# Kernel tuning notes

Measured on AMD Instinct MI355X. Metric: run time of the kernel, lower is better.

## Reference

```python
import jax, jax.numpy as jnp
import numpy as np

B, T, D, H = 32, 2048, 256, 256

def setup_inputs() -> dict:
    key = jax.random.key(0)
    k1, k2, k3 = jax.random.split(key, 3)
    s_x = 1.0 / np.sqrt(D)
    s_h = 1.0 / np.sqrt(H)
    return {
        "x": jax.random.normal(k1, (B, T, D), dtype=jnp.float32),
        "W_x": jax.random.normal(k2, (D, 3 * H), dtype=jnp.float32) * s_x,
        "W_h": jax.random.normal(k3, (H, 3 * H), dtype=jnp.float32) * s_h,
        "b": jnp.zeros((3 * H,), dtype=jnp.float32),
    }

def reference(x, W_x, W_h, b):
    # GRU cell unrolled over time; state starts at zeros (reset_state=True).
    # Precompute input projections for all timesteps in one big GEMM: [B,T,3H]
    x_proj = jnp.einsum("btd,dg->btg", x, W_x) + b
    h0 = jnp.zeros((x.shape[0], H), dtype=x.dtype)

    def step(h, xp_t):
        xz, xr, xn = jnp.split(xp_t, 3, axis=-1)          # each [B,H]
        hz, hr, hn = jnp.split(h @ W_h, 3, axis=-1)        # each [B,H]
        z = jax.nn.sigmoid(xz + hz)
        r = jax.nn.sigmoid(xr + hr)
        n = jnp.tanh(xn + r * hn)
        h_new = z * h + (1.0 - z) * n
        return h_new, h_new

    # scan over time (axis 1 -> move to leading axis)
    _, ys = jax.lax.scan(step, h0, jnp.swapaxes(x_proj, 0, 1))
    return jnp.swapaxes(ys, 0, 1)  # [B,T,H]
```

## Files before the change

kernel.cpp:

```cpp
#include <hip/hip_runtime.h>

#define Bb 32
#define Tt 2048
#define Dd 256
#define Hh 256
#define G3 768

typedef _Float16 h2_t __attribute__((ext_vector_type(2)));
typedef _Float16 f16x8 __attribute__((ext_vector_type(8)));
typedef float f32x4 __attribute__((ext_vector_type(4)));
union H2U { unsigned u; _Float16 h[2]; h2_t v; };
union V16 { uint4 u; f16x8 f; };

__device__ __forceinline__ float fdot2f(unsigned a, unsigned b, float c) {
#if __has_builtin(__builtin_amdgcn_fdot2)
    H2U ua, ub; ua.u = a; ub.u = b;
    return __builtin_amdgcn_fdot2(ua.v, ub.v, c, false);
#else
    H2U ua, ub; ua.u = a; ub.u = b;
    return c + (float)ua.h[0] * (float)ub.h[0] + (float)ua.h[1] * (float)ub.h[1];
#endif
}

__device__ __forceinline__ float frcpf(float x) {
#if __has_builtin(__builtin_amdgcn_rcpf)
    return __builtin_amdgcn_rcpf(x);
#else
    return 1.0f / x;
#endif
}
__device__ __forceinline__ float sigmoidf_(float s) { return frcpf(1.0f + __expf(-s)); }
__device__ __forceinline__ float tanhf_(float u) {
    float e = __expf(2.0f * u);
    return 1.0f - 2.0f * frcpf(e + 1.0f);
}
__device__ __forceinline__ float dpp_xor1(float v) {
    return __int_as_float(__builtin_amdgcn_update_dpp(0, __float_as_int(v), 0xB1, 0xF, 0xF, true));
}
__device__ __forceinline__ float dpp_xor2(float v) {
    return __int_as_float(__builtin_amdgcn_update_dpp(0, __float_as_int(v), 0x4E, 0xF, 0xF, true));
}

__global__ void cvt_x_kernel(const float* __restrict__ x, _Float16* __restrict__ xo) {
    const size_t i = ((size_t)blockIdx.x * 256 + threadIdx.x) * 4;
    float4 v = *reinterpret_cast<const float4*>(x + i);
    H2U a, b;
    a.h[0] = (_Float16)v.x; a.h[1] = (_Float16)v.y;
    b.h[0] = (_Float16)v.z; b.h[1] = (_Float16)v.w;
    uint2 o; o.x = a.u; o.y = b.u;
    *reinterpret_cast<uint2*>(xo + i) = o;
}

__global__ void wxt_kernel(const float* __restrict__ Wx, _Float16* __restrict__ wxt) {
    const int o = blockIdx.x * 256 + threadIdx.x;
    const int n = o >> 7, kp = o & 127;
    float f0 = Wx[(size_t)(2 * kp) * G3 + n];
    float f1 = Wx[(size_t)(2 * kp + 1) * G3 + n];
    H2U u; u.h[0] = (_Float16)f0; u.h[1] = (_Float16)f1;
    reinterpret_cast<unsigned*>(wxt)[o] = u.u;
}

__global__ __launch_bounds__(256)
void gemm_xp_kernel(const _Float16* __restrict__ A, const _Float16* __restrict__ Bm,
                    const float* __restrict__ bias, _Float16* __restrict__ xp) {
    __shared__ _Float16 As[128][264];
    __shared__ _Float16 Bs[64][264];
    const int tid = threadIdx.x;
    const int m0 = (blockIdx.x / 12) * 128;
    const int n0 = (blockIdx.x % 12) * 64;

#pragma unroll
    for (int it = 0; it < 16; ++it) {
        int c = tid + it * 256, row = c >> 5, col = c & 31;
        uint4 v = *reinterpret_cast<const uint4*>(A + (size_t)(m0 + row) * 256 + col * 8);
        *reinterpret_cast<uint4*>(&As[row][col * 8]) = v;
    }
#pragma unroll
    for (int it = 0; it < 8; ++it) {
        int c = tid + it * 256, row = c >> 5, col = c & 31;
        uint4 v = *reinterpret_cast<const uint4*>(Bm + (size_t)(n0 + row) * 256 + col * 8);
        *reinterpret_cast<uint4*>(&Bs[row][col * 8]) = v;
    }
    __syncthreads();

    const int wave = tid >> 6, lane = tid & 63;
    const int wr = wave >> 1, wc = wave & 1;
    const int r16 = lane & 15, kg = lane >> 4;

    f32x4 acc[4][2];
#pragma unroll
    for (int mi = 0; mi < 4; ++mi)
#pragma unroll
        for (int ni = 0; ni < 2; ++ni) acc[mi][ni] = (f32x4){0.f, 0.f, 0.f, 0.f};

    float bv[2];
#pragma unroll
    for (int ni = 0; ni < 2; ++ni) bv[ni] = bias[n0 + wc * 32 + ni * 16 + r16];

#pragma unroll
    for (int kk = 0; kk < 8; ++kk) {
        f16x8 a[4], b2[2];
#pragma unroll
        for (int mi = 0; mi < 4; ++mi) {
            V16 t; t.u = *reinterpret_cast<const uint4*>(&As[wr * 64 + mi * 16 + r16][kk * 32 + kg * 8]);
            a[mi] = t.f;
        }
#pragma unroll
        for (int ni = 0; ni < 2; ++ni) {
            V16 t; t.u = *reinterpret_cast<const uint4*>(&Bs[wc * 32 + ni * 16 + r16][kk * 32 + kg * 8]);
            b2[ni] = t.f;
        }
#pragma unroll
        for (int mi = 0; mi < 4; ++mi)
#pragma unroll
            for (int ni = 0; ni < 2; ++ni)
                acc[mi][ni] = __builtin_amdgcn_mfma_f32_16x16x32_f16(a[mi], b2[ni], acc[mi][ni], 0, 0, 0);
    }

#pragma unroll
    for (int mi = 0; mi < 4; ++mi)
#pragma unroll
        for (int ni = 0; ni < 2; ++ni)
#pragma unroll
            for (int r = 0; r < 4; ++r) {
                int row = m0 + wr * 64 + mi * 16 + kg * 4 + r;
                int col = n0 + wc * 32 + ni * 16 + r16;
                xp[(size_t)row * G3 + col] = (_Float16)(acc[mi][ni][r] + bv[ni]);
            }
}

#define GDOT(HF)                                                                      \
  {                                                                                   \
    uint4 h0 = hq[(HF) * 2 + 0];                                                      \
    uint4 h1 = hq[(HF) * 2 + 1];                                                      \
    _Pragma("unroll") for (int u = 0; u < 4; ++u) {                                   \
      const unsigned hu = (u == 0) ? h0.x : (u == 1) ? h0.y : (u == 2) ? h0.z : h0.w; \
      sz0 = fdot2f(w[0][0][(HF) * 8 + u], hu, sz0);                                   \
      sr0 = fdot2f(w[1][0][(HF) * 8 + u], hu, sr0);                                   \
      sn0 = fdot2f(w[2][0][(HF) * 8 + u], hu, sn0);                                   \
      sz1 = fdot2f(w[0][1][(HF) * 8 + u], hu, sz1);                                   \
      sr1 = fdot2f(w[1][1][(HF) * 8 + u], hu, sr1);                                   \
      sn1 = fdot2f(w[2][1][(HF) * 8 + u], hu, sn1);                                   \
    }                                                                                 \
    _Pragma("unroll") for (int u = 0; u < 4; ++u) {                                   \
      const unsigned hu = (u == 0) ? h1.x : (u == 1) ? h1.y : (u == 2) ? h1.z : h1.w; \
      sz0 = fdot2f(w[0][0][(HF) * 8 + 4 + u], hu, sz0);                               \
      sr0 = fdot2f(w[1][0][(HF) * 8 + 4 + u], hu, sr0);                               \
      sn0 = fdot2f(w[2][0][(HF) * 8 + 4 + u], hu, sn0);                               \
      sz1 = fdot2f(w[0][1][(HF) * 8 + 4 + u], hu, sz1);                               \
      sr1 = fdot2f(w[1][1][(HF) * 8 + 4 + u], hu, sr1);                               \
      sn1 = fdot2f(w[2][1][(HF) * 8 + 4 + u], hu, sn1);                               \
    }                                                                                 \
  }

#define GSTEP(PR, PW, T)                                                              \
  {                                                                                   \
              \
                   \
    const _Float16* xnp = xq + (size_t)((T) + 1 < Tt ? (T) + 1 : (T)) * G3;           \
    _Float16 pz = xnp[0], pr = xnp[Hh], pn = xnp[2 * Hh];                             \
    float sz0 = 0.f, sz1 = 0.f, sr0 = 0.f, sr1 = 0.f, sn0 = 0.f, sn1 = 0.f;           \
    const uint4* hq = reinterpret_cast<const uint4*>(&hbuf[PR][q * 36]);              \
    GDOT(0) GDOT(1) GDOT(2) GDOT(3)                                                   \
                                \
    sz0 += dpp_xor1(sz0); sz1 += dpp_xor1(sz1);                                       \
    sr0 += dpp_xor1(sr0); sr1 += dpp_xor1(sr1);                                       \
    sn0 += dpp_xor1(sn0); sn1 += dpp_xor1(sn1);                                       \
    sz0 += dpp_xor2(sz0); sz1 += dpp_xor2(sz1);                                       \
    sr0 += dpp_xor2(sr0); sr1 += dpp_xor2(sr1);                                       \
    sn0 += dpp_xor2(sn0); sn1 += dpp_xor2(sn1);                                       \
    const float hz = (q & 1) ? sz1 : sz0;                                             \
    const float hr = (q & 1) ? sr1 : sr0;                                             \
    const float hn = (q & 1) ? sn1 : sn0;                                             \
    const float zg = sigmoidf_(xz + hz);                                              \
    const float rg = sigmoidf_(xr + hr);                                              \
    const float ng = tanhf_(xn + rg * hn);                                            \
    const float hnew = zg * hprev + (1.0f - zg) * ng;                                 \
    hprev = hnew;                                                                     \
    H2U hc; hc.h[0] = (_Float16)hnew; hc.h[1] = (_Float16)0.f;                        \
    const unsigned pu = (unsigned)__builtin_amdgcn_update_dpp(0, (int)hc.u, 0xB1, 0xF, 0xF, true); \
    const int pf = __builtin_amdgcn_update_dpp(0, __float_as_int(hnew), 0xB1, 0xF, 0xF, true);      \
    if (q == 0) {                                                                     \
      hbuf[PW][(slot >> 5) * 36 + (slot & 31)] = (hc.u & 0xFFFFu) | (pu << 16);       \
      float2 yv; yv.x = hnew; yv.y = __int_as_float(pf);                              \
      *reinterpret_cast<float2*>(yb + (size_t)(T) * Hh) = yv;                         \
    }                                                                                 \
    xz = (float)pz; xr = (float)pr; xn = (float)pn;                                   \
    __builtin_amdgcn_sched_barrier(0);                                                \
    asm volatile("s_waitcnt lgkmcnt(0)" ::: "memory");                                \
    __builtin_amdgcn_s_barrier();                                                     \
    __builtin_amdgcn_sched_barrier(0);                                                \
  }

__global__ __launch_bounds__(512, 2)
void gru_scan_kernel(const _Float16* __restrict__ xp, const float* __restrict__ Wh,
                     float* __restrict__ y) {
    __shared__ unsigned hbuf[2][144];

    const int tid = threadIdx.x;
    const int b = blockIdx.x;
    const int q = tid & 3;
    const int slot = tid >> 2;

    unsigned w[3][2][32];
#pragma unroll
    for (int g = 0; g < 3; ++g) {
        const int c0 = g * Hh + 2 * slot;
#pragma unroll
        for (int kp = 0; kp < 32; ++kp) {
            const int k = 64 * q + 2 * kp;
            float2 f0 = *reinterpret_cast<const float2*>(Wh + (size_t)k * G3 + c0);
            float2 f1 = *reinterpret_cast<const float2*>(Wh + (size_t)(k + 1) * G3 + c0);
            H2U p0, p1;
            p0.h[0] = (_Float16)f0.x; p0.h[1] = (_Float16)f1.x;
            p1.h[0] = (_Float16)f0.y; p1.h[1] = (_Float16)f1.y;
            w[g][0][kp] = p0.u;
            w[g][1][kp] = p1.u;
        }
    }

    if (tid < 288) hbuf[tid / 144][tid % 144] = 0u;
    float hprev = 0.0f;

    const int j = 2 * slot + (q & 1);
    const _Float16* xq = xp + (size_t)b * Tt * G3 + j;
    float* yb = y + (size_t)b * Tt * Hh + 2 * slot;
    float xz = (float)xq[0], xr = (float)xq[Hh], xn = (float)xq[2 * Hh];

    __syncthreads();

#pragma unroll 1
    for (int t = 0; t < Tt; t += 2) {
        GSTEP(0, 1, t);
        GSTEP(1, 0, t + 1);
    }
}

extern "C" void kernel_launch(void* const* d_in, const int* in_sizes, int n_in,
                              void* d_out, int out_size, void* d_ws, size_t ws_size,
                              hipStream_t stream) {
    (void)in_sizes; (void)n_in; (void)out_size; (void)ws_size;
    const float* x    = (const float*)d_in[0];
    const float* Wx   = (const float*)d_in[1];
    const float* Wh   = (const float*)d_in[2];
    const float* bias = (const float*)d_in[3];
    float* y = (float*)d_out;

    _Float16* xp   = (_Float16*)d_ws;
    _Float16* xf16 = (_Float16*)d_out;
    _Float16* wxt  = (_Float16*)((char*)d_out + (size_t)33554432);

    cvt_x_kernel<<<dim3(16384), dim3(256), 0, stream>>>(x, xf16);
    wxt_kernel<<<dim3(384), dim3(256), 0, stream>>>(Wx, wxt);
    gemm_xp_kernel<<<dim3(6144), dim3(256), 0, stream>>>(xf16, wxt, bias, xp);
    gru_scan_kernel<<<dim3(Bb), dim3(512), 0, stream>>>(xp, Wh, y);
}
```

Baseline: 2.190 ms.

## Halve scan block to 256 threads, each thread computing four hidden columns

The recurrent scan kernel now uses 256 threads per batch row instead of 512. Each thread holds weights for four output columns across all three gates (384 registers), computes 12 partial dot products per step, and owns one hidden unit. This removes the dpp pair exchange for writing h and y and the software prefetch of the next step's input projection. Fewer waves per barrier shortens the per-step synchronisation, but it doubles per-thread FMA work and register pressure, which risks spills and a longer serial step.

Result: slower. 6.281 ms (+186.8%).

```diff
diff --git a/kernel.cpp b/kernel.cpp
--- a/kernel.cpp
+++ b/kernel.cpp
@@ -129,70 +129,60 @@
             }
 }
 
-#define GDOT(HF)                                                                      \
+#define GDCOL(HU, KP)                                                                 \
+    az0 = fdot2f(w[0][0][KP], HU, az0); ar0 = fdot2f(w[1][0][KP], HU, ar0);           \
+    an0 = fdot2f(w[2][0][KP], HU, an0); az1 = fdot2f(w[0][1][KP], HU, az1);           \
+    ar1 = fdot2f(w[1][1][KP], HU, ar1); an1 = fdot2f(w[2][1][KP], HU, an1);           \
+    az2 = fdot2f(w[0][2][KP], HU, az2); ar2 = fdot2f(w[1][2][KP], HU, ar2);           \
+    an2 = fdot2f(w[2][2][KP], HU, an2); az3 = fdot2f(w[0][3][KP], HU, az3);           \
+    ar3 = fdot2f(w[1][3][KP], HU, ar3); an3 = fdot2f(w[2][3][KP], HU, an3);
+
+#define GD4(I)                                                                        \
   {                                                                                   \
-    uint4 h0 = hq[(HF) * 2 + 0];                                                      \
-    uint4 h1 = hq[(HF) * 2 + 1];                                                      \
-    _Pragma("unroll") for (int u = 0; u < 4; ++u) {                                   \
-      const unsigned hu = (u == 0) ? h0.x : (u == 1) ? h0.y : (u == 2) ? h0.z : h0.w; \
-      sz0 = fdot2f(w[0][0][(HF) * 8 + u], hu, sz0);                                   \
-      sr0 = fdot2f(w[1][0][(HF) * 8 + u], hu, sr0);                                   \
-      sn0 = fdot2f(w[2][0][(HF) * 8 + u], hu, sn0);                                   \
-      sz1 = fdot2f(w[0][1][(HF) * 8 + u], hu, sz1);                                   \
-      sr1 = fdot2f(w[1][1][(HF) * 8 + u], hu, sr1);                                   \
-      sn1 = fdot2f(w[2][1][(HF) * 8 + u], hu, sn1);                                   \
-    }                                                                                 \
-    _Pragma("unroll") for (int u = 0; u < 4; ++u) {                                   \
-      const unsigned hu = (u == 0) ? h1.x : (u == 1) ? h1.y : (u == 2) ? h1.z : h1.w; \
-      sz0 = fdot2f(w[0][0][(HF) * 8 + 4 + u], hu, sz0);                               \
-      sr0 = fdot2f(w[1][0][(HF) * 8 + 4 + u], hu, sr0);                               \
-      sn0 = fdot2f(w[2][0][(HF) * 8 + 4 + u], hu, sn0);                               \
-      sz1 = fdot2f(w[0][1][(HF) * 8 + 4 + u], hu, sz1);                               \
-      sr1 = fdot2f(w[1][1][(HF) * 8 + 4 + u], hu, sr1);                               \
-      sn1 = fdot2f(w[2][1][(HF) * 8 + 4 + u], hu, sn1);                               \
-    }                                                                                 \
+    uint4 hv = hq[I];                                                                 \
+    GDCOL(hv.x, (I) * 4 + 0)                                                          \
+    GDCOL(hv.y, (I) * 4 + 1)                                                          \
+    GDCOL(hv.z, (I) * 4 + 2)                                                          \
+    GDCOL(hv.w, (I) * 4 + 3)                                                          \
   }
 
 #define GSTEP(PR, PW, T)                                                              \
   {                                                                                   \
               \
-                   \
-    const _Float16* xnp = xq + (size_t)((T) + 1 < Tt ? (T) + 1 : (T)) * G3;           \
-    _Float16 pz = xnp[0], pr = xnp[Hh], pn = xnp[2 * Hh];                             \
-    float sz0 = 0.f, sz1 = 0.f, sr0 = 0.f, sr1 = 0.f, sn0 = 0.f, sn1 = 0.f;           \
+    const _Float16* xt = xq + (size_t)(T) * G3;                                       \
+    const _Float16 xgz = xt[0], xgr = xt[Hh], xgn = xt[2 * Hh];                       \
+    float az0 = 0.f, az1 = 0.f, az2 = 0.f, az3 = 0.f;                                 \
+    float ar0 = 0.f, ar1 = 0.f, ar2 = 0.f, ar3 = 0.f;                                 \
+    float an0 = 0.f, an1 = 0.f, an2 = 0.f, an3 = 0.f;                                 \
     const uint4* hq = reinterpret_cast<const uint4*>(&hbuf[PR][q * 36]);              \
-    GDOT(0) GDOT(1) GDOT(2) GDOT(3)                                                   \
-                                \
-    sz0 += dpp_xor1(sz0); sz1 += dpp_xor1(sz1);                                       \
-    sr0 += dpp_xor1(sr0); sr1 += dpp_xor1(sr1);                                       \
-    sn0 += dpp_xor1(sn0); sn1 += dpp_xor1(sn1);                                       \
-    sz0 += dpp_xor2(sz0); sz1 += dpp_xor2(sz1);                                       \
-    sr0 += dpp_xor2(sr0); sr1 += dpp_xor2(sr1);                                       \
-    sn0 += dpp_xor2(sn0); sn1 += dpp_xor2(sn1);                                       \
-    const float hz = (q & 1) ? sz1 : sz0;                                             \
-    const float hr = (q & 1) ? sr1 : sr0;                                             \
-    const float hn = (q & 1) ? sn1 : sn0;                                             \
-    const float zg = sigmoidf_(xz + hz);                                              \
-    const float rg = sigmoidf_(xr + hr);                                              \
-    const float ng = tanhf_(xn + rg * hn);                                            \
+    GD4(0) GD4(1) GD4(2) GD4(3) GD4(4) GD4(5) GD4(6) GD4(7)                           \
+    az0 += dpp_xor1(az0); az1 += dpp_xor1(az1); az2 += dpp_xor1(az2);                 \
+    az3 += dpp_xor1(az3); ar0 += dpp_xor1(ar0); ar1 += dpp_xor1(ar1);                 \
+    ar2 += dpp_xor1(ar2); ar3 += dpp_xor1(ar3); an0 += dpp_xor1(an0);                 \
+    an1 += dpp_xor1(an1); an2 += dpp_xor1(an2); an3 += dpp_xor1(an3);                 \
+    az0 += dpp_xor2(az0); az1 += dpp_xor2(az1); az2 += dpp_xor2(az2);                 \
+    az3 += dpp_xor2(az3); ar0 += dpp_xor2(ar0); ar1 += dpp_xor2(ar1);                 \
+    ar2 += dpp_xor2(ar2); ar3 += dpp_xor2(ar3); an0 += dpp_xor2(an0);                 \
+    an1 += dpp_xor2(an1); an2 += dpp_xor2(an2); an3 += dpp_xor2(an3);                 \
+                                     \
+    const float hz = (q & 2) ? ((q & 1) ? az3 : az2) : ((q & 1) ? az1 : az0);         \
+    const float hr = (q & 2) ? ((q & 1) ? ar3 : ar2) : ((q & 1) ? ar1 : ar0);         \
+    const float hn = (q & 2) ? ((q & 1) ? an3 : an2) : ((q & 1) ? an1 : an0);         \
+    const float zg = sigmoidf_((float)xgz + hz);                                      \
+    const float rg = sigmoidf_((float)xgr + hr);                                      \
+    const float ng = tanhf_((float)xgn + rg * hn);                                    \
     const float hnew = zg * hprev + (1.0f - zg) * ng;                                 \
     hprev = hnew;                                                                     \
-    H2U hc; hc.h[0] = (_Float16)hnew; hc.h[1] = (_Float16)0.f;                        \
-    const unsigned pu = (unsigned)__builtin_amdgcn_update_dpp(0, (int)hc.u, 0xB1, 0xF, 0xF, true); \
-    const int pf = __builtin_amdgcn_update_dpp(0, __float_as_int(hnew), 0xB1, 0xF, 0xF, true);      \
-    if (q == 0) {                                                                     \
-      hbuf[PW][(slot >> 5) * 36 + (slot & 31)] = (hc.u & 0xFFFFu) | (pu << 16);       \
-      float2 yv; yv.x = hnew; yv.y = __int_as_float(pf);                              \
-      *reinterpret_cast<float2*>(yb + (size_t)(T) * Hh) = yv;                         \
-    }                                                                                 \
-    xz = (float)pz; xr = (float)pr; xn = (float)pn;                                   \
+    reinterpret_cast<_Float16*>(&hbuf[PW][0])[hoff] = (_Float16)hnew;                 \
+    yb[(size_t)(T) * Hh] = hnew;                                                      \
     __builtin_amdgcn_sched_barrier(0);                                                \
     asm volatile("s_waitcnt lgkmcnt(0)" ::: "memory");                                \
     __builtin_amdgcn_s_barrier();                                                     \
     __builtin_amdgcn_sched_barrier(0);                                                \
   }
 
-__global__ __launch_bounds__(512, 2)
+__global__ __launch_bounds__(256)
+__attribute__((amdgpu_waves_per_eu(1, 1)))
 void gru_scan_kernel(const _Float16* __restrict__ xp, const float* __restrict__ Wh,
                      float* __restrict__ y) {
     __shared__ unsigned hbuf[2][144];
@@ -202,30 +192,30 @@
     const int q = tid & 3;
     const int slot = tid >> 2;
 
-    unsigned w[3][2][32];
-#pragma unroll
-    for (int g = 0; g < 3; ++g) {
-        const int c0 = g * Hh + 2 * slot;
+    unsigned w[3][4][32];
+#pragma unroll
+    for (int g = 0; g < 3; ++g)
 #pragma unroll
         for (int kp = 0; kp < 32; ++kp) {
             const int k = 64 * q + 2 * kp;
-            float2 f0 = *reinterpret_cast<const float2*>(Wh + (size_t)k * G3 + c0);
-            float2 f1 = *reinterpret_cast<const float2*>(Wh + (size_t)(k + 1) * G3 + c0);
-            H2U p0, p1;
-            p0.h[0] = (_Float16)f0.x; p0.h[1] = (_Float16)f1.x;
-            p1.h[0] = (_Float16)f0.y; p1.h[1] = (_Float16)f1.y;
-            w[g][0][kp] = p0.u;
-            w[g][1][kp] = p1.u;
+            const float* p0 = Wh + (size_t)k * G3 + g * Hh + 4 * slot;
+            float4 va = *reinterpret_cast<const float4*>(p0);
+            float4 vb = *reinterpret_cast<const float4*>(p0 + G3);
+            H2U c0, c1, c2, c3;
+            c0.h[0] = (_Float16)va.x; c0.h[1] = (_Float16)vb.x;
+            c1.h[0] = (_Float16)va.y; c1.h[1] = (_Float16)vb.y;
+            c2.h[0] = (_Float16)va.z; c2.h[1] = (_Float16)vb.z;
+            c3.h[0] = (_Float16)va.w; c3.h[1] = (_Float16)vb.w;
+            w[g][0][kp] = c0.u; w[g][1][kp] = c1.u;
+            w[g][2][kp] = c2.u; w[g][3][kp] = c3.u;
         }
-    }
-
-    if (tid < 288) hbuf[tid / 144][tid % 144] = 0u;
+
+    for (int i = tid; i < 288; i += 256) hbuf[i / 144][i % 144] = 0u;
     float hprev = 0.0f;
 
-    const int j = 2 * slot + (q & 1);
-    const _Float16* xq = xp + (size_t)b * Tt * G3 + j;
-    float* yb = y + (size_t)b * Tt * Hh + 2 * slot;
-    float xz = (float)xq[0], xr = (float)xq[Hh], xn = (float)xq[2 * Hh];
+    const int hoff = (tid >> 6) * 72 + (tid & 63);
+    const _Float16* xq = xp + (size_t)b * Tt * G3 + tid;
+    float* yb = y + (size_t)b * Tt * Hh + tid;
 
     __syncthreads();
 
@@ -253,5 +243,5 @@
     cvt_x_kernel<<<dim3(16384), dim3(256), 0, stream>>>(x, xf16);
     wxt_kernel<<<dim3(384), dim3(256), 0, stream>>>(Wx, wxt);
     gemm_xp_kernel<<<dim3(6144), dim3(256), 0, stream>>>(xf16, wxt, bias, xp);
-    gru_scan_kernel<<<dim3(Bb), dim3(512), 0, stream>>>(xp, Wh, y);
-}
+    gru_scan_kernel<<<dim3(Bb), dim3(256), 0, stream>>>(xp, Wh, y);
+}
```

## Split GRU recurrent matvec between VALU dot2 and MFMA with AGPR-pinned weights

Applied to the files above, without the earlier changes.

The recurrent scan now uses 256 threads instead of 512. Half of the hidden columns are computed with fdot2 on VALU using register-resident weights. The other half use MFMA 16x16x32 with W_h fragments pinned in AGPRs and the h vector broadcast as the A operand. This is meant to cut the per-step VALU dot-product latency by overlapping matrix-core and vector work, and to reduce barrier cost with fewer waves. In exchange, MFMA computes 16 redundant rows, register pressure is high, and correctness depends on the new fragment layout.

New measurement: 3.630 ms. 65.8% more time.

```diff
diff --git a/kernel.cpp b/kernel.cpp
--- a/kernel.cpp
+++ b/kernel.cpp
@@ -40,6 +40,11 @@
 __device__ __forceinline__ float dpp_xor2(float v) {
     return __int_as_float(__builtin_amdgcn_update_dpp(0, __float_as_int(v), 0x4E, 0xF, 0xF, true));
 }
+__device__ __forceinline__ f16x8 agpr_pin(f16x8 v) {
+    f16x8 r;
+    asm("" : "=a"(r) : "0"(v));
+    return r;
+}
 
 __global__ void cvt_x_kernel(const float* __restrict__ x, _Float16* __restrict__ xo) {
     const size_t i = ((size_t)blockIdx.x * 256 + threadIdx.x) * 4;
@@ -129,83 +134,121 @@
             }
 }
 
-#define GDOT(HF)                                                                      \
+#define GKT(PR, KT)                                                                   \
   {                                                                                   \
-    uint4 h0 = hq[(HF) * 2 + 0];                                                      \
-    uint4 h1 = hq[(HF) * 2 + 1];                                                      \
-    _Pragma("unroll") for (int u = 0; u < 4; ++u) {                                   \
-      const unsigned hu = (u == 0) ? h0.x : (u == 1) ? h0.y : (u == 2) ? h0.z : h0.w; \
-      sz0 = fdot2f(w[0][0][(HF) * 8 + u], hu, sz0);                                   \
-      sr0 = fdot2f(w[1][0][(HF) * 8 + u], hu, sr0);                                   \
-      sn0 = fdot2f(w[2][0][(HF) * 8 + u], hu, sn0);                                   \
-      sz1 = fdot2f(w[0][1][(HF) * 8 + u], hu, sz1);                                   \
-      sr1 = fdot2f(w[1][1][(HF) * 8 + u], hu, sr1);                                   \
-      sn1 = fdot2f(w[2][1][(HF) * 8 + u], hu, sn1);                                   \
-    }                                                                                 \
-    _Pragma("unroll") for (int u = 0; u < 4; ++u) {                                   \
-      const unsigned hu = (u == 0) ? h1.x : (u == 1) ? h1.y : (u == 2) ? h1.z : h1.w; \
-      sz0 = fdot2f(w[0][0][(HF) * 8 + 4 + u], hu, sz0);                               \
-      sr0 = fdot2f(w[1][0][(HF) * 8 + 4 + u], hu, sr0);                               \
-      sn0 = fdot2f(w[2][0][(HF) * 8 + 4 + u], hu, sn0);                               \
-      sz1 = fdot2f(w[0][1][(HF) * 8 + 4 + u], hu, sz1);                               \
-      sr1 = fdot2f(w[1][1][(HF) * 8 + 4 + u], hu, sr1);                               \
-      sn1 = fdot2f(w[2][1][(HF) * 8 + 4 + u], hu, sn1);                               \
-    }                                                                                 \
+    V16 af_; af_.u = *reinterpret_cast<const uint4*>(                                 \
+        reinterpret_cast<const char*>(&hbuf[PR][0]) + (KT) * 64 + kg * 16);           \
+    uint4 hv = *reinterpret_cast<const uint4*>(                                       \
+        reinterpret_cast<const char*>(&hbuf[PR][0]) + q * 128 + (KT) * 16);           \
+    az_a = __builtin_amdgcn_mfma_f32_16x16x32_f16(af_.f, bf[0][0][KT], az_a, 0, 0, 0); \
+    vz0 = fdot2f(w[0][0][4 * (KT) + 0], hv.x, vz0);                                   \
+    vz1 = fdot2f(w[0][1][4 * (KT) + 0], hv.x, vz1);                                   \
+    vr0 = fdot2f(w[1][0][4 * (KT) + 0], hv.x, vr0);                                   \
+    vr1 = fdot2f(w[1][1][4 * (KT) + 0], hv.x, vr1);                                   \
+    az_b = __builtin_amdgcn_mfma_f32_16x16x32_f16(af_.f, bf[0][1][KT], az_b, 0, 0, 0); \
+    vn0 = fdot2f(w[2][0][4 * (KT) + 0], hv.x, vn0);                                   \
+    vn1 = fdot2f(w[2][1][4 * (KT) + 0], hv.x, vn1);                                   \
+    vz0 = fdot2f(w[0][0][4 * (KT) + 1], hv.y, vz0);                                   \
+    vz1 = fdot2f(w[0][1][4 * (KT) + 1], hv.y, vz1);                                   \
+    ar_a = __builtin_amdgcn_mfma_f32_16x16x32_f16(af_.f, bf[1][0][KT], ar_a, 0, 0, 0); \
+    vr0 = fdot2f(w[1][0][4 * (KT) + 1], hv.y, vr0);                                   \
+    vr1 = fdot2f(w[1][1][4 * (KT) + 1], hv.y, vr1);                                   \
+    vn0 = fdot2f(w[2][0][4 * (KT) + 1], hv.y, vn0);                                   \
+    vn1 = fdot2f(w[2][1][4 * (KT) + 1], hv.y, vn1);                                   \
+    ar_b = __builtin_amdgcn_mfma_f32_16x16x32_f16(af_.f, bf[1][1][KT], ar_b, 0, 0, 0); \
+    vz0 = fdot2f(w[0][0][4 * (KT) + 2], hv.z, vz0);                                   \
+    vz1 = fdot2f(w[0][1][4 * (KT) + 2], hv.z, vz1);                                   \
+    vr0 = fdot2f(w[1][0][4 * (KT) + 2], hv.z, vr0);                                   \
+    vr1 = fdot2f(w[1][1][4 * (KT) + 2], hv.z, vr1);                                   \
+    an_a = __builtin_amdgcn_mfma_f32_16x16x32_f16(af_.f, bf[2][0][KT], an_a, 0, 0, 0); \
+    vn0 = fdot2f(w[2][0][4 * (KT) + 2], hv.z, vn0);                                   \
+    vn1 = fdot2f(w[2][1][4 * (KT) + 2], hv.z, vn1);                                   \
+    vz0 = fdot2f(w[0][0][4 * (KT) + 3], hv.w, vz0);                                   \
+    vz1 = fdot2f(w[0][1][4 * (KT) + 3], hv.w, vz1);                                   \
+    an_b = __builtin_amdgcn_mfma_f32_16x16x32_f16(af_.f, bf[2][1][KT], an_b, 0, 0, 0); \
+    vr0 = fdot2f(w[1][0][4 * (KT) + 3], hv.w, vr0);                                   \
+    vr1 = fdot2f(w[1][1][4 * (KT) + 3], hv.w, vr1);                                   \
+    vn0 = fdot2f(w[2][0][4 * (KT) + 3], hv.w, vn0);                                   \
+    vn1 = fdot2f(w[2][1][4 * (KT) + 3], hv.w, vn1);                                   \
   }
 
 #define GSTEP(PR, PW, T)                                                              \
   {                                                                                   \
-              \
-                   \
-    const _Float16* xnp = xq + (size_t)((T) + 1 < Tt ? (T) + 1 : (T)) * G3;           \
-    _Float16 pz = xnp[0], pr = xnp[Hh], pn = xnp[2 * Hh];                             \
-    float sz0 = 0.f, sz1 = 0.f, sr0 = 0.f, sr1 = 0.f, sn0 = 0.f, sn1 = 0.f;           \
-    const uint4* hq = reinterpret_cast<const uint4*>(&hbuf[PR][q * 36]);              \
-    GDOT(0) GDOT(1) GDOT(2) GDOT(3)                                                   \
-                                \
-    sz0 += dpp_xor1(sz0); sz1 += dpp_xor1(sz1);                                       \
-    sr0 += dpp_xor1(sr0); sr1 += dpp_xor1(sr1);                                       \
-    sn0 += dpp_xor1(sn0); sn1 += dpp_xor1(sn1);                                       \
-    sz0 += dpp_xor2(sz0); sz1 += dpp_xor2(sz1);                                       \
-    sr0 += dpp_xor2(sr0); sr1 += dpp_xor2(sr1);                                       \
-    sn0 += dpp_xor2(sn0); sn1 += dpp_xor2(sn1);                                       \
-    const float hz = (q & 1) ? sz1 : sz0;                                             \
-    const float hr = (q & 1) ? sr1 : sr0;                                             \
-    const float hn = (q & 1) ? sn1 : sn0;                                             \
-    const float zg = sigmoidf_(xz + hz);                                              \
-    const float rg = sigmoidf_(xr + hr);                                              \
-    const float ng = tanhf_(xn + rg * hn);                                            \
-    const float hnew = zg * hprev + (1.0f - zg) * ng;                                 \
-    hprev = hnew;                                                                     \
-    H2U hc; hc.h[0] = (_Float16)hnew; hc.h[1] = (_Float16)0.f;                        \
-    const unsigned pu = (unsigned)__builtin_amdgcn_update_dpp(0, (int)hc.u, 0xB1, 0xF, 0xF, true); \
-    const int pf = __builtin_amdgcn_update_dpp(0, __float_as_int(hnew), 0xB1, 0xF, 0xF, true);      \
+                \
+    unsigned xvz = 0u, xvr = 0u, xvn = 0u;                                            \
+    _Float16 xmz = (_Float16)0.f, xmr = (_Float16)0.f, xmn = (_Float16)0.f;           \
     if (q == 0) {                                                                     \
-      hbuf[PW][(slot >> 5) * 36 + (slot & 31)] = (hc.u & 0xFFFFu) | (pu << 16);       \
-      float2 yv; yv.x = hnew; yv.y = __int_as_float(pf);                              \
-      *reinterpret_cast<float2*>(yb + (size_t)(T) * Hh) = yv;                         \
+      const _Float16* xt = xpv + (size_t)(T) * G3;                                    \
+      xvz = *reinterpret_cast<const unsigned*>(xt);                                   \
+      xvr = *reinterpret_cast<const unsigned*>(xt + Hh);                              \
+      xvn = *reinterpret_cast<const unsigned*>(xt + 2 * Hh);                          \
     }                                                                                 \
-    xz = (float)pz; xr = (float)pr; xn = (float)pn;                                   \
+    if (lane < 32) {                                                                  \
+      const _Float16* xt = xpm + (size_t)(T) * G3;                                    \
+      xmz = xt[0]; xmr = xt[Hh]; xmn = xt[2 * Hh];                                    \
+    }                                                                                 \
+    f32x4 az_a = {0.f, 0.f, 0.f, 0.f}, az_b = {0.f, 0.f, 0.f, 0.f};                   \
+    f32x4 ar_a = {0.f, 0.f, 0.f, 0.f}, ar_b = {0.f, 0.f, 0.f, 0.f};                   \
+    f32x4 an_a = {0.f, 0.f, 0.f, 0.f}, an_b = {0.f, 0.f, 0.f, 0.f};                   \
+    float vz0 = 0.f, vz1 = 0.f, vr0 = 0.f, vr1 = 0.f, vn0 = 0.f, vn1 = 0.f;           \
+    GKT(PR, 0) GKT(PR, 1) GKT(PR, 2) GKT(PR, 3)                                       \
+    GKT(PR, 4) GKT(PR, 5) GKT(PR, 6) GKT(PR, 7)                                       \
+    vz0 += dpp_xor1(vz0); vz1 += dpp_xor1(vz1);                                       \
+    vr0 += dpp_xor1(vr0); vr1 += dpp_xor1(vr1);                                       \
+    vn0 += dpp_xor1(vn0); vn1 += dpp_xor1(vn1);                                       \
+    vz0 += dpp_xor2(vz0); vz1 += dpp_xor2(vz1);                                       \
+    vr0 += dpp_xor2(vr0); vr1 += dpp_xor2(vr1);                                       \
+    vn0 += dpp_xor2(vn0); vn1 += dpp_xor2(vn1);                                       \
+    if (q == 0) {                                                                     \
+      H2U uz, ur, un; uz.u = xvz; ur.u = xvr; un.u = xvn;                             \
+      float z0 = sigmoidf_((float)uz.h[0] + vz0);                                     \
+      float r0 = sigmoidf_((float)ur.h[0] + vr0);                                     \
+      float n0 = tanhf_((float)un.h[0] + r0 * vn0);                                   \
+      float hn0 = z0 * hv_prev0 + (1.0f - z0) * n0;                                   \
+      float z1 = sigmoidf_((float)uz.h[1] + vz1);                                     \
+      float r1 = sigmoidf_((float)ur.h[1] + vr1);                                     \
+      float n1 = tanhf_((float)un.h[1] + r1 * vn1);                                   \
+      float hn1 = z1 * hv_prev1 + (1.0f - z1) * n1;                                   \
+      hv_prev0 = hn0; hv_prev1 = hn1;                                                 \
+      H2U hp; hp.h[0] = (_Float16)hn0; hp.h[1] = (_Float16)hn1;                       \
+      hbuf[PW][16 * wv + s] = hp.u;                                                   \
+      float2 yv; yv.x = hn0; yv.y = hn1;                                              \
+      *reinterpret_cast<float2*>(ybv + (size_t)(T) * Hh) = yv;                        \
+    }                                                                                 \
+    if (lane < 32) {                                                                  \
+      float mz = (lane & 16) ? az_b[0] : az_a[0];                                     \
+      float mr = (lane & 16) ? ar_b[0] : ar_a[0];                                     \
+      float mn = (lane & 16) ? an_b[0] : an_a[0];                                     \
+      float zg = sigmoidf_((float)xmz + mz);                                          \
+      float rg = sigmoidf_((float)xmr + mr);                                          \
+      float ng = tanhf_((float)xmn + rg * mn);                                        \
+      float hm = zg * hm_prev + (1.0f - zg) * ng;                                     \
+      hm_prev = hm;                                                                   \
+      reinterpret_cast<_Float16*>(&hbuf[PW][0])[jm] = (_Float16)hm;                   \
+      ybm[(size_t)(T) * Hh] = hm;                                                     \
+    }                                                                                 \
     __builtin_amdgcn_sched_barrier(0);                                                \
     asm volatile("s_waitcnt lgkmcnt(0)" ::: "memory");                                \
     __builtin_amdgcn_s_barrier();                                                     \
     __builtin_amdgcn_sched_barrier(0);                                                \
   }
 
-__global__ __launch_bounds__(512, 2)
+__global__ __launch_bounds__(256)
+__attribute__((amdgpu_waves_per_eu(1, 1)))
 void gru_scan_kernel(const _Float16* __restrict__ xp, const float* __restrict__ Wh,
                      float* __restrict__ y) {
-    __shared__ unsigned hbuf[2][144];
+    __shared__ unsigned hbuf[2][128];
 
     const int tid = threadIdx.x;
     const int b = blockIdx.x;
-    const int q = tid & 3;
-    const int slot = tid >> 2;
+    const int wv = tid >> 6, lane = tid & 63;
+    const int q = lane & 3, s = lane >> 2;
+    const int r16 = lane & 15, kg = lane >> 4;
 
     unsigned w[3][2][32];
 #pragma unroll
     for (int g = 0; g < 3; ++g) {
-        const int c0 = g * Hh + 2 * slot;
+        const int c0 = g * Hh + 32 * wv + 2 * s;
 #pragma unroll
         for (int kp = 0; kp < 32; ++kp) {
             const int k = 64 * q + 2 * kp;
@@ -219,13 +262,31 @@
         }
     }
 
-    if (tid < 288) hbuf[tid / 144][tid % 144] = 0u;
-    float hprev = 0.0f;
-
-    const int j = 2 * slot + (q & 1);
-    const _Float16* xq = xp + (size_t)b * Tt * G3 + j;
-    float* yb = y + (size_t)b * Tt * Hh + 2 * slot;
-    float xz = (float)xq[0], xr = (float)xq[Hh], xn = (float)xq[2 * Hh];
+    f16x8 bf[3][2][8];
+#pragma unroll
+    for (int g = 0; g < 3; ++g)
+#pragma unroll
+        for (int w2 = 0; w2 < 2; ++w2)
+#pragma unroll
+            for (int kt = 0; kt < 8; ++kt) {
+                V16 t;
+#pragma unroll
+                for (int j = 0; j < 8; ++j) {
+                    const int k = 32 * kt + 8 * kg + j;
+                    t.f[j] = (_Float16)Wh[(size_t)k * G3 + g * Hh + 128 + 32 * wv + 16 * w2 + r16];
+                }
+                bf[g][w2][kt] = agpr_pin(t.f);
+            }
+
+    if (tid < 128) hbuf[0][tid] = 0u;
+    float hv_prev0 = 0.f, hv_prev1 = 0.f, hm_prev = 0.f;
+
+    const int jv = 32 * wv + 2 * s;
+    const int jm = 128 + 32 * wv + (lane & 31);
+    const _Float16* xpv = xp + (size_t)b * Tt * G3 + jv;
+    const _Float16* xpm = xp + (size_t)b * Tt * G3 + jm;
+    float* ybv = y + (size_t)b * Tt * Hh + jv;
+    float* ybm = y + (size_t)b * Tt * Hh + jm;
 
     __syncthreads();
 
@@ -253,5 +314,5 @@
     cvt_x_kernel<<<dim3(16384), dim3(256), 0, stream>>>(x, xf16);
     wxt_kernel<<<dim3(384), dim3(256), 0, stream>>>(Wx, wxt);
     gemm_xp_kernel<<<dim3(6144), dim3(256), 0, stream>>>(xf16, wxt, bias, xp);
-    gru_scan_kernel<<<dim3(Bb), dim3(512), 0, stream>>>(xp, Wh, y);
-}
+    gru_scan_kernel<<<dim3(Bb), dim3(256), 0, stream>>>(xp, Wh, y);
+}
```
